# Kernel optimization log

Measured on AMD Instinct MI355X. Metric: run time of the kernel, lower is better.

Reference implementation:

```python
import jax, jax.numpy as jnp
import numpy as np

SCALE = 2
STRIDE = 1


def setup_inputs() -> dict:
    key = jax.random.key(0)
    k1, k2 = jax.random.split(key)
    feature = jax.random.normal(k1, (8, 32, 160, 160), dtype=jnp.float32)
    # depthwise dynamic kernel: ksize^2 * scale^2 = 9 * 4 = 36 channels per pixel
    kernel = jax.random.normal(k2, (8, 36, 160, 160), dtype=jnp.float32)
    return {"feature": feature, "kernel": kernel}


def reference(feature, kernel):
    # PixelConv(scale=2, depthwise=True, stride=1)
    N, C, H, W = feature.shape
    S2 = SCALE * SCALE
    ks = int(round((kernel.shape[1] // S2) ** 0.5))  # 3
    pad = (ks - 1) // 2
    padded = jnp.pad(feature, ((0, 0), (0, 0), (pad, pad), (pad, pad)))
    # torch does unfold(H).unfold(W) then permute(...,5,4): flattened patch
    # index is dx*ks + dy (width-offset major). Replicate that ordering.
    patches = jnp.stack(
        [padded[:, :, dy:dy + H, dx:dx + W] for dx in range(ks) for dy in range(ks)],
        axis=-1,
    )  # [N, C, H, W, ks*ks]
    # kernel: [N, ks*ks*S2, H, W] -> [N, H, W, ks*ks, S2]
    kr = kernel.transpose(0, 2, 3, 1).reshape(N, H, W, ks * ks, S2)
    # per-pixel matmul, kernel shared across channels (depthwise)
    out = jnp.einsum('nchwk,nhwks->ncshw', patches, kr)  # [N, C, S2, H, W]
    out = out.reshape(N, C * S2, H, W)
    # pixel_shuffle(scale)
    r = SCALE
    out = out.reshape(N, C, r, r, H, W).transpose(0, 1, 4, 2, 5, 3)
    return out.reshape(N, C, H * r, W * r)
```

## Files before the change

kernel.cpp:

```cpp
#include <hip/hip_runtime.h>

#define HH 160
#define WW 160
#define CC 32
#define NN 8
#define PIX (HH * WW)

typedef float f32x2 __attribute__((ext_vector_type(2)));

__global__ __launch_bounds__(640, 5) void pixelconv_k(
    const float* __restrict__ feature,
    const float* __restrict__ kern,
    float* __restrict__ out)
{
    const int bx = blockIdx.x;
    const int h  = (bx & 7) * 20 + (bx >> 3);
    const int n  = blockIdx.y;
    const int t  = threadIdx.x;
    const int wl = t % 160;
    const int cg = t / 160;

    __shared__ float kv_lds[36 * 160];
    const float* kbase = kern + (size_t)n * 36 * PIX + (size_t)h * WW;
    #pragma unroll
    for (int r = 0; r < 9; ++r) {
        const int idx = t + r * 640;
        const int j   = idx / 160;
        const int ws  = idx - j * 160;
        kv_lds[idx] = kbase[(size_t)j * PIX + ws];
    }
    __syncthreads();

    float kv[36];
    #pragma unroll
    for (int j = 0; j < 36; ++j) kv[j] = kv_lds[j * 160 + wl];

    const bool hm = (h > 0), hp = (h < HH - 1);
    const bool wm = (wl > 0), wp = (wl < WW - 1);

    const float* fc = feature + ((size_t)(n * CC + cg * 8)) * PIX
                              + (size_t)h * WW + wl;
    float* oc = out + ((size_t)(n * CC + cg * 8)) * 4 * PIX
                    + (size_t)(2 * h) * (2 * WW) + 2 * wl;

    #pragma unroll 2
    for (int i = 0; i < 8; ++i) {
        float f[9];
        #pragma unroll
        for (int dx = 0; dx < 3; ++dx) {
            #pragma unroll
            for (int dy = 0; dy < 3; ++dy) {
                const bool ok = (dy != 0 || hm) && (dy != 2 || hp) &&
                                (dx != 0 || wm) && (dx != 2 || wp);
                f[dx * 3 + dy] = ok ? fc[(dy - 1) * WW + (dx - 1)] : 0.0f;
            }
        }

        float a0 = 0.f, a1 = 0.f, a2 = 0.f, a3 = 0.f;
        #pragma unroll
        for (int k = 0; k < 9; ++k) {
            a0 = fmaf(f[k], kv[4 * k + 0], a0);
            a1 = fmaf(f[k], kv[4 * k + 1], a1);
            a2 = fmaf(f[k], kv[4 * k + 2], a2);
            a3 = fmaf(f[k], kv[4 * k + 3], a3);
        }

        *(f32x2*)(oc)          = (f32x2){a0, a1};
        *(f32x2*)(oc + 2 * WW) = (f32x2){a2, a3};

        fc += PIX;
        oc += (size_t)4 * PIX;
    }
}

extern "C" void kernel_launch(void* const* d_in, const int* in_sizes, int n_in,
                              void* d_out, int out_size, void* d_ws, size_t ws_size,
                              hipStream_t stream) {
    const float* feature = (const float*)d_in[0];
    const float* kern    = (const float*)d_in[1];
    float* out           = (float*)d_out;

    dim3 grid(HH, NN, 1);
    pixelconv_k<<<grid, 640, 0, stream>>>(feature, kern, out);
}
```

Before: 32.34 us.

## Compute two adjacent pixels per thread with vectorized loads and 16-byte stores

```diff
diff --git a/kernel.cpp b/kernel.cpp
--- a/kernel.cpp
+++ b/kernel.cpp
@@ -7,8 +7,9 @@
 #define PIX (HH * WW)
 
 typedef float f32x2 __attribute__((ext_vector_type(2)));
+typedef float f32x4 __attribute__((ext_vector_type(4)));
 
-__global__ __launch_bounds__(640, 5) void pixelconv_k(
+__global__ __launch_bounds__(640, 4) void pixelconv_k(
     const float* __restrict__ feature,
     const float* __restrict__ kern,
     float* __restrict__ out)
@@ -17,8 +18,9 @@
     const int h  = (bx & 7) * 20 + (bx >> 3);
     const int n  = blockIdx.y;
     const int t  = threadIdx.x;
-    const int wl = t % 160;
-    const int cg = t / 160;
+    const int p  = t % 80;
+    const int cg = t / 80;
+    const int w0 = 2 * p;
 
     __shared__ float kv_lds[36 * 160];
     const float* kbase = kern + (size_t)n * 36 * PIX + (size_t)h * WW;
@@ -31,42 +33,54 @@
     }
     __syncthreads();
 
-    float kv[36];
+    f32x2 kv[36];
     #pragma unroll
-    for (int j = 0; j < 36; ++j) kv[j] = kv_lds[j * 160 + wl];
+    for (int j = 0; j < 36; ++j) kv[j] = *(const f32x2*)&kv_lds[j * 160 + w0];
 
     const bool hm = (h > 0), hp = (h < HH - 1);
-    const bool wm = (wl > 0), wp = (wl < WW - 1);
+    const bool wm = (p > 0), wp = (p < 79);
 
-    const float* fc = feature + ((size_t)(n * CC + cg * 8)) * PIX
-                              + (size_t)h * WW + wl;
-    float* oc = out + ((size_t)(n * CC + cg * 8)) * 4 * PIX
-                    + (size_t)(2 * h) * (2 * WW) + 2 * wl;
+    const float* fc = feature + ((size_t)(n * CC + cg * 4)) * PIX
+                              + (size_t)h * WW + w0;
+    float* oc = out + ((size_t)(n * CC + cg * 4)) * 4 * PIX
+                    + (size_t)(2 * h) * (2 * WW) + 2 * w0;
 
-    #pragma unroll 2
-    for (int i = 0; i < 8; ++i) {
-        float f[9];
+    #pragma unroll
+    for (int i = 0; i < 4; ++i) {
+        float r[3][4];
+        #pragma unroll
+        for (int dy = 0; dy < 3; ++dy) {
+            const bool okh = (dy == 1) || (dy == 0 ? hm : hp);
+            const float* rowp = fc + (dy - 1) * WW;
+            f32x2 mid = okh ? *(const f32x2*)rowp : (f32x2){0.f, 0.f};
+            r[dy][1] = mid.x;
+            r[dy][2] = mid.y;
+            r[dy][0] = (okh && wm) ? rowp[-1] : 0.f;
+            r[dy][3] = (okh && wp) ? rowp[2]  : 0.f;
+        }
+
+        float a00 = 0.f, a01 = 0.f, a02 = 0.f, a03 = 0.f;
+        float a10 = 0.f, a11 = 0.f, a12 = 0.f, a13 = 0.f;
         #pragma unroll
         for (int dx = 0; dx < 3; ++dx) {
             #pragma unroll
             for (int dy = 0; dy < 3; ++dy) {
-                const bool ok = (dy != 0 || hm) && (dy != 2 || hp) &&
-                                (dx != 0 || wm) && (dx != 2 || wp);
-                f[dx * 3 + dy] = ok ? fc[(dy - 1) * WW + (dx - 1)] : 0.0f;
+                const int k = dx * 3 + dy;
+                const float f0 = r[dy][dx];
+                const float f1 = r[dy][dx + 1];
+                a00 = fmaf(f0, kv[4 * k + 0].x, a00);
+                a01 = fmaf(f0, kv[4 * k + 1].x, a01);
+                a02 = fmaf(f0, kv[4 * k + 2].x, a02);
+                a03 = fmaf(f0, kv[4 * k + 3].x, a03);
+                a10 = fmaf(f1, kv[4 * k + 0].y, a10);
+                a11 = fmaf(f1, kv[4 * k + 1].y, a11);
+                a12 = fmaf(f1, kv[4 * k + 2].y, a12);
+                a13 = fmaf(f1, kv[4 * k + 3].y, a13);
             }
         }
 
-        float a0 = 0.f, a1 = 0.f, a2 = 0.f, a3 = 0.f;
-        #pragma unroll
-        for (int k = 0; k < 9; ++k) {
-            a0 = fmaf(f[k], kv[4 * k + 0], a0);
-            a1 = fmaf(f[k], kv[4 * k + 1], a1);
-            a2 = fmaf(f[k], kv[4 * k + 2], a2);
-            a3 = fmaf(f[k], kv[4 * k + 3], a3);
-        }
-
-        *(f32x2*)(oc)          = (f32x2){a0, a1};
-        *(f32x2*)(oc + 2 * WW) = (f32x2){a2, a3};
+        *(f32x4*)(oc)          = (f32x4){a00, a01, a10, a11};
+        *(f32x4*)(oc + 2 * WW) = (f32x4){a02, a03, a12, a13};
 
         fc += PIX;
         oc += (size_t)4 * PIX;
```

Measured after the change: 53.52 us. 1.65x slower.

## Stage padded feature halo rows in LDS in two channel halves

Applied to the files above, without the earlier changes.

```diff
diff --git a/kernel.cpp b/kernel.cpp
--- a/kernel.cpp
+++ b/kernel.cpp
@@ -5,10 +5,11 @@
 #define CC 32
 #define NN 8
 #define PIX (HH * WW)
+#define COLS 168
 
 typedef float f32x2 __attribute__((ext_vector_type(2)));
 
-__global__ __launch_bounds__(640, 5) void pixelconv_k(
+__global__ __launch_bounds__(640) void pixelconv_k(
     const float* __restrict__ feature,
     const float* __restrict__ kern,
     float* __restrict__ out)
@@ -21,6 +22,8 @@
     const int cg = t / 160;
 
     __shared__ float kv_lds[36 * 160];
+    __shared__ float ft_lds[48 * COLS];
+
     const float* kbase = kern + (size_t)n * 36 * PIX + (size_t)h * WW;
     #pragma unroll
     for (int r = 0; r < 9; ++r) {
@@ -29,47 +32,74 @@
         const int ws  = idx - j * 160;
         kv_lds[idx] = kbase[(size_t)j * PIX + ws];
     }
-    __syncthreads();
 
     float kv[36];
-    #pragma unroll
-    for (int j = 0; j < 36; ++j) kv[j] = kv_lds[j * 160 + wl];
+    const bool kvload[1] = {};
+    (void)kvload;
 
-    const bool hm = (h > 0), hp = (h < HH - 1);
-    const bool wm = (wl > 0), wp = (wl < WW - 1);
+    #pragma unroll 1
+    for (int half = 0; half < 2; ++half) {
+        const int c0 = half * 16;
 
-    const float* fc = feature + ((size_t)(n * CC + cg * 8)) * PIX
-                              + (size_t)h * WW + wl;
-    float* oc = out + ((size_t)(n * CC + cg * 8)) * 4 * PIX
-                    + (size_t)(2 * h) * (2 * WW) + 2 * wl;
-
-    #pragma unroll 2
-    for (int i = 0; i < 8; ++i) {
-        float f[9];
+        const float* fb = feature + ((size_t)(n * CC + c0)) * PIX;
         #pragma unroll
-        for (int dx = 0; dx < 3; ++dx) {
-            #pragma unroll
-            for (int dy = 0; dy < 3; ++dy) {
-                const bool ok = (dy != 0 || hm) && (dy != 2 || hp) &&
-                                (dx != 0 || wm) && (dx != 2 || wp);
-                f[dx * 3 + dy] = ok ? fc[(dy - 1) * WW + (dx - 1)] : 0.0f;
+        for (int it = 0; it < 13; ++it) {
+            const int idx = t + it * 640;
+            if (idx < 48 * 162) {
+                const int row = idx / 162;
+                const int col = idx - row * 162;
+                const int ch  = row / 3;
+                const int dy  = row - ch * 3;
+                const int hh  = h + dy - 1;
+                const int w   = col - 1;
+                float v = 0.f;
+                if ((unsigned)hh < HH && (unsigned)w < WW)
+                    v = fb[(size_t)ch * PIX + (size_t)hh * WW + w];
+                ft_lds[row * COLS + col] = v;
             }
         }
+        __syncthreads();
 
-        float a0 = 0.f, a1 = 0.f, a2 = 0.f, a3 = 0.f;
-        #pragma unroll
-        for (int k = 0; k < 9; ++k) {
-            a0 = fmaf(f[k], kv[4 * k + 0], a0);
-            a1 = fmaf(f[k], kv[4 * k + 1], a1);
-            a2 = fmaf(f[k], kv[4 * k + 2], a2);
-            a3 = fmaf(f[k], kv[4 * k + 3], a3);
+        if (half == 0) {
+            #pragma unroll
+            for (int j = 0; j < 36; ++j) kv[j] = kv_lds[j * 160 + wl];
         }
 
-        *(f32x2*)(oc)          = (f32x2){a0, a1};
-        *(f32x2*)(oc + 2 * WW) = (f32x2){a2, a3};
+        float* oc = out + ((size_t)(n * CC + c0 + cg * 4)) * 4 * PIX
+                        + (size_t)(2 * h) * (2 * WW) + 2 * wl;
 
-        fc += PIX;
-        oc += (size_t)4 * PIX;
+        #pragma unroll 2
+        for (int i = 0; i < 4; ++i) {
+            const int chl = cg * 4 + i;
+            const float* fr = &ft_lds[(chl * 3) * COLS + wl];
+
+            float r0[3], r1[3], r2[3];
+            #pragma unroll
+            for (int j = 0; j < 3; ++j) {
+                r0[j] = fr[j];
+                r1[j] = fr[COLS + j];
+                r2[j] = fr[2 * COLS + j];
+            }
+
+            float a0 = 0.f, a1 = 0.f, a2 = 0.f, a3 = 0.f;
+            #pragma unroll
+            for (int dx = 0; dx < 3; ++dx) {
+                #pragma unroll
+                for (int dy = 0; dy < 3; ++dy) {
+                    const int k = dx * 3 + dy;
+                    const float f = (dy == 0) ? r0[dx] : (dy == 1) ? r1[dx] : r2[dx];
+                    a0 = fmaf(f, kv[4 * k + 0], a0);
+                    a1 = fmaf(f, kv[4 * k + 1], a1);
+                    a2 = fmaf(f, kv[4 * k + 2], a2);
+                    a3 = fmaf(f, kv[4 * k + 3], a3);
+                }
+            }
+
+            *(f32x2*)(oc)          = (f32x2){a0, a1};
+            *(f32x2*)(oc + 2 * WW) = (f32x2){a2, a3};
+            oc += (size_t)4 * PIX;
+        }
+        __syncthreads();
     }
 }
 
```

Result: slower. 57.48 us (+77.7%).
